# Performance work log

Hardware: AMD Instinct MI355X
Metric: run time of the kernel (lower is better)

The kernel has to match this reference:

```python
import jax, jax.numpy as jnp
import numpy as np

T = 48; S = 48; H = 250; EMB = 300; VOCAB = 50000; NL = 5


def setup_inputs():
    key = jax.random.key(0)
    ks = jax.random.split(key, 32)
    def rn(k, shape, scale=0.05):
        return jax.random.normal(k, shape, dtype=jnp.float32) * scale
    return {
        "x1": jax.random.randint(ks[0], (T,), 0, VOCAB),
        "x2": jax.random.randint(ks[1], (S,), 0, VOCAB),
        "emb": rn(ks[2], (VOCAB, EMB), 1.0),
        "w_ih_f": rn(ks[3], (4 * H, EMB)),
        "w_hh_f": rn(ks[4], (4 * H, H)),
        "b_f": rn(ks[5], (4 * H,)),
        "w_ih_b": rn(ks[6], (4 * H, EMB)),
        "w_hh_b": rn(ks[7], (4 * H, H)),
        "b_b": rn(ks[8], (4 * H,)),
        "c1_w": rn(ks[9], (128, 13, 3, 3)),  "c1_b": rn(ks[10], (128,)),
        "c2_w": rn(ks[11], (164, 128, 3, 3)), "c2_b": rn(ks[12], (164,)),
        "c3_w": rn(ks[13], (192, 164, 3, 3)), "c3_b": rn(ks[14], (192,)),
        "c4_w": rn(ks[15], (192, 192, 3, 3)), "c4_b": rn(ks[16], (192,)),
        "c5_w": rn(ks[17], (128, 192, 3, 3)), "c5_b": rn(ks[18], (128,)),
        "dnn_w": rn(ks[19], (128, 128)), "dnn_b": rn(ks[20], (128,)),
        "out_w": rn(ks[21], (NL, 128)), "out_b": rn(ks[22], (NL,)),
    }


def _lstm_dir(xW, w_hh, b, reverse):
    # xW: [T, 4H] precomputed input projection
    def cell(carry, g_in):
        h, c = carry
        g = g_in + h @ w_hh.T + b
        i, f, gg, o = jnp.split(g, 4)
        i = jax.nn.sigmoid(i); f = jax.nn.sigmoid(f)
        gg = jnp.tanh(gg); o = jax.nn.sigmoid(o)
        c = f * c + i * gg
        h = o * jnp.tanh(c)
        return (h, c), h
    h0 = jnp.zeros((w_hh.shape[1],), xW.dtype)
    _, hs = jax.lax.scan(cell, (h0, h0), xW, reverse=reverse)
    return hs  # [T, H], aligned to input positions


def _bilstm(x, w_ih_f, w_hh_f, b_f, w_ih_b, w_hh_b, b_b):
    hf = _lstm_dir(x @ w_ih_f.T, w_hh_f, b_f, False)
    hb = _lstm_dir(x @ w_ih_b.T, w_hh_b, b_b, True)
    return jnp.stack([hf, hb], axis=1)  # [T, 2, H]


def _sim(a, b):
    # a:[T,D], b:[S,D] -> [3,T,S] channels (dot, cos, l2) -- fully batched
    dot = a @ b.T
    na = jnp.sqrt(jnp.sum(a * a, -1))
    nb = jnp.sqrt(jnp.sum(b * b, -1))
    cos = dot / (na[:, None] * nb[None, :] + 1e-8)
    d2 = jnp.maximum(na[:, None] ** 2 + nb[None, :] ** 2 - 2.0 * dot, 1e-12)
    l2 = jnp.sqrt(d2)
    return jnp.stack([dot, cos, l2], 0)


def _sim_cube(seq1, seq2):
    h1f, h1b = seq1[:, 0], seq1[:, 1]
    h2f, h2b = seq2[:, 0], seq2[:, 1]
    parts = [
        _sim(jnp.concatenate([h1f, h1b], -1), jnp.concatenate([h2f, h2b], -1)),
        _sim(h1f, h2f),
        _sim(h1b, h2b),
        _sim(h1f + h1b, h2f + h2b),
    ]
    pad = jnp.zeros((1, seq1.shape[0], seq2.shape[0]), seq1.dtype)  # channel 12
    return jnp.concatenate(parts + [pad], 0)  # [13, T, S]


def _greedy_select(plane):
    # greedy non-conflicting pair selection over top (T+S) entries
    t, s = plane.shape
    _, idx = jax.lax.top_k(plane.reshape(-1), t + s)
    def step(carry, i):
        s1, s2, m = carry
        p1 = i // t  # faithful to original (divides by len(s1tag))
        p2 = i % s
        ok = (s1[p1] + s2[p2]) == 0
        s1 = s1.at[p1].set(jnp.where(ok, 1, s1[p1]))
        s2 = s2.at[p2].set(jnp.where(ok, 1, s2[p2]))
        m = m.at[p1, p2].set(m[p1, p2] | ok)
        return (s1, s2, m), None
    init = (jnp.zeros(t, jnp.int32), jnp.zeros(s, jnp.int32), jnp.zeros((t, s), bool))
    (_, _, m), _ = jax.lax.scan(step, init, idx)
    return m


def _focus_cube(sc):
    sel = _greedy_select(sc[10]) | _greedy_select(sc[11])
    mask = jnp.where(sel[None], 1.0, 0.1).astype(sc.dtype)  # 0.1 base per VDPWI
    mask = mask.at[12].set(1.0)
    return mask * sc


def _convnet(x, c1_w, c1_b, c2_w, c2_b, c3_w, c3_b, c4_w, c4_b, c5_w, c5_b,
             dnn_w, dnn_b, out_w, out_b):
    def conv(x, w, b):
        y = jax.lax.conv_general_dilated(
            x, w, (1, 1), ((1, 1), (1, 1)),
            dimension_numbers=("NCHW", "OIHW", "NCHW"))
        return y + b[None, :, None, None]
    def pool(x, k, st):
        return jax.lax.reduce_window(
            x, -jnp.inf, jax.lax.max, (1, 1, k, k), (1, 1, st, st), "VALID")
    x = pool(jax.nn.relu(conv(x, c1_w, c1_b)), 2, 2)  # 48->24
    x = pool(jax.nn.relu(conv(x, c2_w, c2_b)), 2, 2)  # 24->12
    x = pool(jax.nn.relu(conv(x, c3_w, c3_b)), 2, 2)  # 12->6
    x = pool(jax.nn.relu(conv(x, c4_w, c4_b)), 2, 2)  # 6->3
    x = pool(jax.nn.relu(conv(x, c5_w, c5_b)), 3, 1)  # 3->1
    x = x.reshape(x.shape[0], -1)  # [1, 128]
    x = jax.nn.relu(x @ dnn_w.T + dnn_b)
    return x @ out_w.T + out_b


def reference(x1, x2, emb, w_ih_f, w_hh_f, b_f, w_ih_b, w_hh_b, b_b,
              c1_w, c1_b, c2_w, c2_b, c3_w, c3_b, c4_w, c4_b, c5_w, c5_b,
              dnn_w, dnn_b, out_w, out_b):
    e1 = emb[x1]  # [T, 300]
    e2 = emb[x2]  # [S, 300]
    seq1 = _bilstm(e1, w_ih_f, w_hh_f, b_f, w_ih_b, w_hh_b, b_b)
    seq2 = _bilstm(e2, w_ih_f, w_hh_f, b_f, w_ih_b, w_hh_b, b_b)
    sc = _sim_cube(seq1, seq2)        # [13, T, S]
    fc = _focus_cube(sc)
    logits = _convnet(fc[None], c1_w, c1_b, c2_w, c2_b, c3_w, c3_b,
                      c4_w, c4_b, c5_w, c5_b, dnn_w, dnn_b, out_w, out_b)
    return jax.nn.log_softmax(logits, axis=-1)
```

## Files before the change

kernel.cpp:

```cpp
#include <hip/hip_runtime.h>
#include <math.h>


typedef __attribute__((ext_vector_type(2))) _Float16 h2f;
typedef unsigned long long u64;

#define OFF_XW    0
#define OFF_HS    192000
#define OFF_SC    240000
#define OFF_BUFA  269952
#define OFF_BUFB  343680
#define OFF_WIHT  367296
#define OFF_WPK   967296
#define OFF_SEL   1217296

__device__ __forceinline__ float sigf(float x) { return 1.f / (1.f + expf(-x)); }

#if __has_builtin(__builtin_amdgcn_fdot2)
__device__ __forceinline__ float dot2(h2f a, h2f b, float c) {
    return __builtin_amdgcn_fdot2(a, b, c, false);
}
#else
__device__ __forceinline__ float dot2(h2f a, h2f b, float c) {
    return c + (float)a.x * (float)b.x + (float)a.y * (float)b.y;
}
#endif

__global__ void prep_kernel(const float* __restrict__ wihf, const float* __restrict__ wihb,
                            const float* __restrict__ whhf, const float* __restrict__ whhb,
                            float* __restrict__ wT, unsigned int* __restrict__ wpk)
{
    if (blockIdx.z < 2) {
        __shared__ float tile[32][33];
        int dir = blockIdx.z;
        const float* w = dir ? wihb : wihf;

        int j = blockIdx.x * 32 + threadIdx.y;
        int k = blockIdx.y * 32 + threadIdx.x;
        if (j < 1000 && k < 300)
            tile[threadIdx.y][threadIdx.x] = w[(size_t)j * 300 + k];
        __syncthreads();

        int ko = blockIdx.y * 32 + threadIdx.y;
        int jo = blockIdx.x * 32 + threadIdx.x;
        if (ko < 300 && jo < 1000)
            wT[(size_t)dir * 300000 + (size_t)ko * 1000 + jo] = tile[threadIdx.x][threadIdx.y];
    } else {
        if (blockIdx.y >= 8) return;
        __shared__ unsigned int ptile[32][33];
        int jt  = blockIdx.x;
        int pt  = blockIdx.y & 3;
        int dir = blockIdx.y >> 2;
        const float* w = dir ? whhb : whhf;

        int p = pt * 32 + threadIdx.x;
        int j = jt * 32 + threadIdx.y;
        if (p < 125 && j < 1000) {
            float2 v = *(const float2*)(w + (size_t)j * 250 + 2 * p);
            h2f pv; pv.x = (_Float16)v.x; pv.y = (_Float16)v.y;
            ptile[threadIdx.y][threadIdx.x] = *(unsigned int*)&pv;
        }
        __syncthreads();

        int jo = jt * 32 + threadIdx.x;
        int po = pt * 32 + threadIdx.y;
        if (po < 125 && jo < 1000)
            wpk[(size_t)dir * 125000 + (size_t)po * 1000 + jo] = ptile[threadIdx.x][threadIdx.y];
    }
}

__global__ void embed_xw_kernel(const int* __restrict__ x1, const int* __restrict__ x2,
                                const float* __restrict__ emb, const float* __restrict__ wT,
                                const float* __restrict__ b_f, const float* __restrict__ b_b,
                                float* __restrict__ xW)
{
    int t = blockIdx.x % 48;
    int m = blockIdx.x / 48;
    const int* x = (m < 2) ? x1 : x2;
    const float* w = wT + (size_t)(m & 1) * 300000;
    const float* bias = (m & 1) ? b_b : b_f;

    __shared__ float e[300];
    int row = x[t];
    for (int k = threadIdx.x; k < 300; k += 512)
        e[k] = emb[(size_t)row * 300 + k];
    __syncthreads();

    int j0 = threadIdx.x;
    int j1 = threadIdx.x + 512;
    int j1c = j1 < 1000 ? j1 : 999;
    float a0 = 0.f, a1 = 0.f;
    #pragma unroll 4
    for (int k = 0; k < 300; ++k) {
        float ek = e[k];
        const float* wr = w + (size_t)k * 1000;
        a0 += ek * wr[j0];
        a1 += ek * wr[j1c];
    }
    float* out = xW + ((size_t)m * 48 + t) * 1000;
    out[j0] = a0 + bias[j0];
    if (j1 < 1000) out[j1] = a1 + bias[j1];
}

__global__ void __launch_bounds__(512, 1) lstm_kernel(
    const float* __restrict__ xW, const unsigned int* __restrict__ wpk,
    float* __restrict__ hs)
{
    int m   = blockIdx.x;
    int dir = m & 1;
    const unsigned int* wp = wpk + (size_t)dir * 125000;
    const float* xw = xW + (size_t)m * 48000;
    float* out      = hs + (size_t)m * 12000;

    int t = threadIdx.x;
    bool active = t < 500;
    int r0 = t, r1 = t + 500;

    __shared__ __align__(16) unsigned int hp[128];
    __shared__ float fo_lds[500];
    __shared__ __align__(16) uint4 wl4[3 * 1000];

    for (int idx = t; idx < 3000; idx += 512) {
        int q = idx / 1000, r = idx % 1000;
        uint4 v;
        v.x = wp[(4 * q + 0) * 1000 + r];
        v.y = wp[(4 * q + 1) * 1000 + r];
        v.z = wp[(4 * q + 2) * 1000 + r];
        v.w = wp[(4 * q + 3) * 1000 + r];
        wl4[idx] = v;
    }

    h2f w0r[113], w1r[113];
    if (active) {
        #pragma unroll
        for (int p = 0; p < 113; ++p) {
            unsigned int a = wp[(p + 12) * 1000 + r0];
            unsigned int b = wp[(p + 12) * 1000 + r1];
            w0r[p] = *(h2f*)&a;
            w1r[p] = *(h2f*)&b;
        }
    }
    if (t < 128) hp[t] = 0u;
    float c = 0.f;

    int tt = dir ? 47 : 0;
    float px0 = 0.f, px1 = 0.f;
    if (active) {
        px0 = xw[tt * 1000 + r0];
        px1 = xw[tt * 1000 + r1];
    }
    __syncthreads();

    for (int step = 0; step < 48; ++step) {
        int ttn = dir ? 46 - step : step + 1;
        float n0 = 0.f, n1 = 0.f;
        if (active && step < 47) {
            n0 = xw[ttn * 1000 + r0];
            n1 = xw[ttn * 1000 + r1];
        }
        float a0 = 0.f, a1 = 0.f;
        if (active) {
            float a0e = px0, a0o = 0.f, a1e = px1, a1o = 0.f;
            const uint4* hp4 = (const uint4*)hp;
            #pragma unroll
            for (int q = 0; q < 3; ++q) {
                uint4 hq = hp4[q];
                h2f h0 = *(h2f*)&hq.x, h1 = *(h2f*)&hq.y, h2v = *(h2f*)&hq.z, h3 = *(h2f*)&hq.w;
                uint4 wv0 = wl4[q * 1000 + r0];
                uint4 wv1 = wl4[q * 1000 + r1];
                a0e = dot2(*(h2f*)&wv0.x, h0, a0e);  a1e = dot2(*(h2f*)&wv1.x, h0, a1e);
                a0o = dot2(*(h2f*)&wv0.y, h1, a0o);  a1o = dot2(*(h2f*)&wv1.y, h1, a1o);
                a0e = dot2(*(h2f*)&wv0.z, h2v, a0e); a1e = dot2(*(h2f*)&wv1.z, h2v, a1e);
                a0o = dot2(*(h2f*)&wv0.w, h3, a0o);  a1o = dot2(*(h2f*)&wv1.w, h3, a1o);
            }
            #pragma unroll
            for (int jj = 3; jj < 31; ++jj) {
                uint4 hq = hp4[jj];
                h2f h0 = *(h2f*)&hq.x, h1 = *(h2f*)&hq.y, h2v = *(h2f*)&hq.z, h3 = *(h2f*)&hq.w;
                int p = 4 * jj - 12;
                a0e = dot2(w0r[p + 0], h0, a0e);  a1e = dot2(w1r[p + 0], h0, a1e);
                a0o = dot2(w0r[p + 1], h1, a0o);  a1o = dot2(w1r[p + 1], h1, a1o);
                a0e = dot2(w0r[p + 2], h2v, a0e); a1e = dot2(w1r[p + 2], h2v, a1e);
                a0o = dot2(w0r[p + 3], h3, a0o);  a1o = dot2(w1r[p + 3], h3, a1o);
            }
            {
                unsigned int hq = hp[124];
                h2f hv = *(h2f*)&hq;
                a0e = dot2(w0r[112], hv, a0e);
                a1e = dot2(w1r[112], hv, a1e);
            }
            a0 = a0e + a0o;
            a1 = a1e + a1o;
            if (t >= 250) {
                fo_lds[t - 250] = sigf(a0);
                fo_lds[250 + (t - 250)] = sigf(a1);
            }
        }
        __syncthreads();
        if (t < 250) {
            float iv = sigf(a0);
            float gv = tanhf(a1);
            float fv = fo_lds[t];
            float ov = fo_lds[250 + t];
            c = fv * c + iv * gv;
            float hn = ov * tanhf(c);
            out[tt * 250 + t] = hn;
            float hi = __shfl_down(hn, 1);
            if (!(t & 1)) {
                h2f pv; pv.x = (_Float16)hn; pv.y = (_Float16)hi;
                hp[t >> 1] = *(unsigned int*)&pv;
            }
        }
        px0 = n0; px1 = n1; tt = ttn;
        __syncthreads();
    }
}

__global__ void sim_kernel(const float* __restrict__ hs, float* __restrict__ sc)
{
    int p = blockIdx.x;
    int i = p / 48, jj = p % 48;
    const float* h1f = hs + ((size_t)0 * 48 + i) * 250;
    const float* h1b = hs + ((size_t)1 * 48 + i) * 250;
    const float* h2f = hs + ((size_t)2 * 48 + jj) * 250;
    const float* h2b = hs + ((size_t)3 * 48 + jj) * 250;
    int lane = threadIdx.x;
    float dff = 0.f, dbb = 0.f, dfb = 0.f, dbf = 0.f;
    float sfa = 0.f, sba = 0.f, caa = 0.f;
    float sfb = 0.f, sbb = 0.f, cbb = 0.f;
    for (int k = lane; k < 250; k += 64) {
        float af = h1f[k], ab = h1b[k], bf = h2f[k], bb = h2b[k];
        dff += af * bf; dbb += ab * bb; dfb += af * bb; dbf += ab * bf;
        sfa += af * af; sba += ab * ab; caa += af * ab;
        sfb += bf * bf; sbb += bb * bb; cbb += bf * bb;
    }
    #pragma unroll
    for (int o = 32; o; o >>= 1) {
        dff += __shfl_down(dff, o); dbb += __shfl_down(dbb, o);
        dfb += __shfl_down(dfb, o); dbf += __shfl_down(dbf, o);
        sfa += __shfl_down(sfa, o); sba += __shfl_down(sba, o);
        caa += __shfl_down(caa, o);
        sfb += __shfl_down(sfb, o); sbb += __shfl_down(sbb, o);
        cbb += __shfl_down(cbb, o);
    }
    if (lane == 0) {
        #define EMIT(basep, dotv, sa2, sb2)                                 \
        {                                                                   \
            float na = sqrtf(sa2), nbv = sqrtf(sb2);                        \
            float dv = (dotv);                                              \
            sc[(basep) * 2304 + p] = dv;                                    \
            sc[((basep) + 1) * 2304 + p] = dv / (na * nbv + 1e-8f);         \
            float d2 = fmaxf(na * na + nbv * nbv - 2.f * dv, 1e-12f);       \
            sc[((basep) + 2) * 2304 + p] = sqrtf(d2);                       \
        }
        EMIT(0, dff + dbb, sfa + sba, sfb + sbb);
        EMIT(3, dff, sfa, sfb);
        EMIT(6, dbb, sba, sbb);
        EMIT(9, dff + dfb + dbf + dbb, sfa + sba + 2.f * caa, sfb + sbb + 2.f * cbb);
        #undef EMIT
    }
}

__global__ void greedy_kernel(const float* __restrict__ sc, unsigned char* __restrict__ sel)
{
    __shared__ unsigned char selL[2304];
    int lane = threadIdx.x;
    int plane = 10 + blockIdx.x;

    u64 v[36];
    #pragma unroll
    for (int q = 0; q < 36; ++q) {
        int i = lane + 64 * q;
        unsigned int u = __float_as_uint(sc[plane * 2304 + i]);
        unsigned int ord = (u & 0x80000000u) ? ~u : (u | 0x80000000u);
        v[q] = ((u64)ord << 32) | (unsigned int)(4095 - i);
        selL[i] = 0;
    }

    #pragma unroll
    for (int a = 0; a < 35; ++a) {
        #pragma unroll
        for (int b = 0; b < 35 - a; ++b) {
            u64 lo = v[b] < v[b + 1] ? v[b] : v[b + 1];
            u64 hi = v[b] < v[b + 1] ? v[b + 1] : v[b];
            v[b] = hi; v[b + 1] = lo;
        }
    }
    __syncthreads();

    u64 m1 = 0, m2 = 0;
    for (int it = 0; it < 96; ++it) {
        u64 bv = v[0];
        #pragma unroll
        for (int o = 1; o < 64; o <<= 1) {
            u64 ov = __shfl_xor(bv, o);
            if (ov > bv) bv = ov;
        }
        int idx = 4095 - (int)(bv & 0xFFFFFFFFu);
        int p1 = idx / 48, p2 = idx % 48;
        bool ok = !((m1 >> p1) & 1) && !((m2 >> p2) & 1);
        if (ok) { m1 |= 1ull << p1; m2 |= 1ull << p2; }
        if (v[0] == bv) {
            if (ok) selL[idx] = 1;
            #pragma unroll
            for (int q = 0; q < 35; ++q) v[q] = v[q + 1];
            v[35] = 0;
        }
    }
    __syncthreads();
    for (int q = 0; q < 36; ++q) {
        int i = lane + 64 * q;
        sel[blockIdx.x * 2304 + i] = selL[i];
    }
}

__global__ void conv1_pool_kernel(const float* __restrict__ sc, const unsigned char* __restrict__ sel,
                                  const float* __restrict__ w, const float* __restrict__ bias,
                                  float* __restrict__ out)
{
    __shared__ float tile[256];
    int co  = blockIdx.x / 9;
    int tl  = blockIdx.x % 9;
    int ty0 = (tl / 3) * 16, tx0 = (tl % 3) * 16;
    int tx = threadIdx.x % 16, ty = threadIdx.x / 16;
    int x = tx0 + tx, y = ty0 + ty;

    float mv[9];
    #pragma unroll
    for (int ky = 0; ky < 3; ++ky) {
        int iy = y + ky - 1;
        #pragma unroll
        for (int kx = 0; kx < 3; ++kx) {
            int ix = x + kx - 1;
            float mm = 0.f;
            if (iy >= 0 && iy < 48 && ix >= 0 && ix < 48) {
                int p = iy * 48 + ix;
                mm = (sel[p] | sel[2304 + p]) ? 1.0f : 0.1f;
            }
            mv[ky * 3 + kx] = mm;
        }
    }

    float acc = bias[co];
    const float* wco = w + (size_t)co * 13 * 9;
    for (int ci = 0; ci < 12; ++ci) {
        const float* inp = sc + (size_t)ci * 2304;
        const float* wp = wco + ci * 9;
        #pragma unroll
        for (int ky = 0; ky < 3; ++ky) {
            int iy = y + ky - 1;
            if (iy < 0 || iy >= 48) continue;
            #pragma unroll
            for (int kx = 0; kx < 3; ++kx) {
                int ix = x + kx - 1;
                if (ix < 0 || ix >= 48) continue;
                acc += inp[iy * 48 + ix] * mv[ky * 3 + kx] * wp[ky * 3 + kx];
            }
        }
    }
    tile[threadIdx.x] = acc > 0.f ? acc : 0.f;
    __syncthreads();
    if (threadIdx.x < 64) {
        int py = threadIdx.x / 8, px = threadIdx.x % 8;
        float a = tile[(py * 2) * 16 + px * 2];
        float b = tile[(py * 2) * 16 + px * 2 + 1];
        float cc = tile[(py * 2 + 1) * 16 + px * 2];
        float d = tile[(py * 2 + 1) * 16 + px * 2 + 1];
        float best = fmaxf(fmaxf(a, b), fmaxf(cc, d));
        out[(size_t)co * 576 + (ty0 / 2 + py) * 24 + (tx0 / 2 + px)] = best;
    }
}

__global__ void conv_cs_kernel(const float* __restrict__ in, const float* __restrict__ w,
                               const float* __restrict__ bias, float* __restrict__ out,
                               int Cin, int H, int W, int tileH, int tileW,
                               int cpc, int CC, int pk, int ps, int PHf, int PWf)
{
    extern __shared__ float sm[];
    int P = tileH * tileW;
    int co = blockIdx.x;
    int ty0 = blockIdx.y * tileH, tx0 = blockIdx.z * tileW;
    int t = threadIdx.x;
    int pix = t % P, chunk = t / P;
    int y = ty0 + pix / tileW, x = tx0 + pix % tileW;
    int c0 = chunk * cpc;
    int c1 = c0 + cpc; if (c1 > Cin) c1 = Cin;

    float acc = 0.f;
    const float* wco = w + (size_t)co * Cin * 9;
    for (int ci = c0; ci < c1; ++ci) {
        const float* inp = in + (size_t)ci * H * W;
        const float* wp = wco + (size_t)ci * 9;
        #pragma unroll
        for (int ky = 0; ky < 3; ++ky) {
            int iy = y + ky - 1;
            if (iy < 0 || iy >= H) continue;
            const float* rowp = inp + iy * W;
            #pragma unroll
            for (int kx = 0; kx < 3; ++kx) {
                int ix = x + kx - 1;
                if (ix < 0 || ix >= W) continue;
                acc += rowp[ix] * wp[ky * 3 + kx];
            }
        }
    }
    sm[t] = acc;
    __syncthreads();
    float* res = sm + P * CC;
    if (chunk == 0) {
        float tot = bias[co];
        for (int cc2 = 0; cc2 < CC; ++cc2) tot += sm[pix + cc2 * P];
        res[pix] = tot > 0.f ? tot : 0.f;
    }
    __syncthreads();
    int pH = (tileH - pk) / ps + 1, pW = (tileW - pk) / ps + 1;
    if (t < pH * pW) {
        int py = t / pW, px = t % pW;
        float best = -INFINITY;
        for (int dy = 0; dy < pk; ++dy)
            for (int dx = 0; dx < pk; ++dx) {
                float v = res[(py * ps + dy) * tileW + (px * ps + dx)];
                best = v > best ? v : best;
            }
        out[((size_t)co * PHf + (ty0 / ps + py)) * PWf + (tx0 / ps + px)] = best;
    }
}

__global__ void head_kernel(const float* __restrict__ feat,
                            const float* __restrict__ dnn_w, const float* __restrict__ dnn_b,
                            const float* __restrict__ out_w, const float* __restrict__ out_b,
                            float* __restrict__ out)
{
    __shared__ float y[128];
    __shared__ float logits[5];
    int j = threadIdx.x;
    float acc = dnn_b[j];
    for (int k = 0; k < 128; ++k) acc += feat[k] * dnn_w[j * 128 + k];
    y[j] = acc > 0.f ? acc : 0.f;
    __syncthreads();
    if (j < 5) {
        float a = out_b[j];
        for (int k = 0; k < 128; ++k) a += y[k] * out_w[j * 128 + k];
        logits[j] = a;
    }
    __syncthreads();
    if (j == 0) {
        float m = logits[0];
        for (int l = 1; l < 5; ++l) m = fmaxf(m, logits[l]);
        float s = 0.f;
        for (int l = 0; l < 5; ++l) s += expf(logits[l] - m);
        float lse = logf(s);
        for (int l = 0; l < 5; ++l) out[l] = logits[l] - m - lse;
    }
}

extern "C" void kernel_launch(void* const* d_in, const int* in_sizes, int n_in,
                              void* d_out, int out_size, void* d_ws, size_t ws_size,
                              hipStream_t stream)
{
    const int*   x1     = (const int*)d_in[0];
    const int*   x2     = (const int*)d_in[1];
    const float* emb    = (const float*)d_in[2];
    const float* w_ih_f = (const float*)d_in[3];
    const float* w_hh_f = (const float*)d_in[4];
    const float* b_f    = (const float*)d_in[5];
    const float* w_ih_b = (const float*)d_in[6];
    const float* w_hh_b = (const float*)d_in[7];
    const float* b_b    = (const float*)d_in[8];
    const float* c1_w   = (const float*)d_in[9];
    const float* c1_b   = (const float*)d_in[10];
    const float* c2_w   = (const float*)d_in[11];
    const float* c2_b   = (const float*)d_in[12];
    const float* c3_w   = (const float*)d_in[13];
    const float* c3_b   = (const float*)d_in[14];
    const float* c4_w   = (const float*)d_in[15];
    const float* c4_b   = (const float*)d_in[16];
    const float* c5_w   = (const float*)d_in[17];
    const float* c5_b   = (const float*)d_in[18];
    const float* dnn_w  = (const float*)d_in[19];
    const float* dnn_b  = (const float*)d_in[20];
    const float* out_w  = (const float*)d_in[21];
    const float* out_b  = (const float*)d_in[22];

    float* ws    = (float*)d_ws;
    float* xW    = ws + OFF_XW;
    float* hsb   = ws + OFF_HS;
    float* sc    = ws + OFF_SC;
    float* bufA  = ws + OFF_BUFA;
    float* bufB  = ws + OFF_BUFB;
    float* wihT  = ws + OFF_WIHT;
    unsigned int* wpk = (unsigned int*)(ws + OFF_WPK);
    unsigned char* sel = (unsigned char*)(ws + OFF_SEL);
    float* outp  = (float*)d_out;

    prep_kernel<<<dim3(32, 10, 3), dim3(32, 32), 0, stream>>>(
        w_ih_f, w_ih_b, w_hh_f, w_hh_b, wihT, wpk);
    embed_xw_kernel<<<192, 512, 0, stream>>>(x1, x2, emb, wihT, b_f, b_b, xW);
    lstm_kernel<<<4, 512, 0, stream>>>(xW, wpk, hsb);
    sim_kernel<<<2304, 64, 0, stream>>>(hsb, sc);
    greedy_kernel<<<2, 64, 0, stream>>>(sc, sel);

    conv1_pool_kernel<<<128 * 9, 256, 0, stream>>>(sc, sel, c1_w, c1_b, bufA);
    conv_cs_kernel<<<dim3(164, 2, 2), 576, (576 + 144) * 4, stream>>>(
        bufA, c2_w, c2_b, bufB, 128, 24, 24, 12, 12, 32, 4, 2, 2, 12, 12);
    conv_cs_kernel<<<dim3(192, 1, 1), 576, (576 + 144) * 4, stream>>>(
        bufB, c3_w, c3_b, bufA, 164, 12, 12, 12, 12, 41, 4, 2, 2, 6, 6);
    conv_cs_kernel<<<dim3(192, 1, 1), 576, (576 + 36) * 4, stream>>>(
        bufA, c4_w, c4_b, bufB, 192, 6, 6, 6, 6, 12, 16, 2, 2, 3, 3);
    conv_cs_kernel<<<dim3(128, 1, 1), 576, (576 + 9) * 4, stream>>>(
        bufB, c5_w, c5_b, bufA, 192, 3, 3, 3, 3, 3, 64, 3, 1, 1, 1);

    head_kernel<<<1, 128, 0, stream>>>(bufA, dnn_w, dnn_b, out_w, out_b, outp);
}
```

Baseline: 345.6 us.

## Fuse sim, greedy, conv stack and head into one persistent kernel with grid barriers

Eight separate launches (similarity, greedy matching, five conv/pool layers, head) become a single persistent kernel of 256 blocks. The stages are separated by atomic-counter grid barriers, and the counter is reset in prep_kernel. The aim is to remove per-launch overhead and the gaps between the many tiny kernels that follow the LSTM. In exchange, the greedy stage runs while most blocks spin at a barrier, and correctness depends on all 256 blocks being co-resident.

```diff
diff --git a/kernel.cpp b/kernel.cpp
--- a/kernel.cpp
+++ b/kernel.cpp
@@ -13,6 +13,9 @@
 #define OFF_WIHT  367296
 #define OFF_WPK   967296
 #define OFF_SEL   1217296
+#define OFF_CNT   1218448
+
+#define NBLK 256
 
 __device__ __forceinline__ float sigf(float x) { return 1.f / (1.f + expf(-x)); }
 
@@ -26,10 +29,28 @@
 }
 #endif
 
+__device__ __forceinline__ void gridbar(int* cnt, int target) {
+    __syncthreads();
+    if (threadIdx.x == 0) {
+        __hip_atomic_fetch_add(cnt, 1, __ATOMIC_ACQ_REL, __HIP_MEMORY_SCOPE_AGENT);
+        while (__hip_atomic_load(cnt, __ATOMIC_ACQUIRE, __HIP_MEMORY_SCOPE_AGENT) < target) {
+#if __has_builtin(__builtin_amdgcn_s_sleep)
+            __builtin_amdgcn_s_sleep(2);
+#endif
+        }
+    }
+    __syncthreads();
+}
+
 __global__ void prep_kernel(const float* __restrict__ wihf, const float* __restrict__ wihb,
                             const float* __restrict__ whhf, const float* __restrict__ whhb,
-                            float* __restrict__ wT, unsigned int* __restrict__ wpk)
+                            float* __restrict__ wT, unsigned int* __restrict__ wpk,
+                            int* __restrict__ cnt)
 {
+    if (blockIdx.x == 0 && blockIdx.y == 0 && blockIdx.z == 0 &&
+        threadIdx.x == 0 && threadIdx.y == 0)
+        __hip_atomic_store(cnt, 0, __ATOMIC_RELAXED, __HIP_MEMORY_SCOPE_AGENT);
+
     if (blockIdx.z < 2) {
         __shared__ float tile[32][33];
         int dir = blockIdx.z;
@@ -216,241 +237,270 @@
     }
 }
 
-__global__ void sim_kernel(const float* __restrict__ hs, float* __restrict__ sc)
+__device__ __forceinline__ void conv_tile(const float* __restrict__ in, const float* __restrict__ w,
+    const float* __restrict__ bias, float* __restrict__ out, float* sm, int t, bool act,
+    int Cin, int H, int W, int tileH, int tileW, int ty0, int tx0,
+    int cpc, int CC, int pk, int ps, int PHf, int PWf, int co)
 {
-    int p = blockIdx.x;
-    int i = p / 48, jj = p % 48;
-    const float* h1f = hs + ((size_t)0 * 48 + i) * 250;
-    const float* h1b = hs + ((size_t)1 * 48 + i) * 250;
-    const float* h2f = hs + ((size_t)2 * 48 + jj) * 250;
-    const float* h2b = hs + ((size_t)3 * 48 + jj) * 250;
-    int lane = threadIdx.x;
-    float dff = 0.f, dbb = 0.f, dfb = 0.f, dbf = 0.f;
-    float sfa = 0.f, sba = 0.f, caa = 0.f;
-    float sfb = 0.f, sbb = 0.f, cbb = 0.f;
-    for (int k = lane; k < 250; k += 64) {
-        float af = h1f[k], ab = h1b[k], bf = h2f[k], bb = h2b[k];
-        dff += af * bf; dbb += ab * bb; dfb += af * bb; dbf += ab * bf;
-        sfa += af * af; sba += ab * ab; caa += af * ab;
-        sfb += bf * bf; sbb += bb * bb; cbb += bf * bb;
-    }
-    #pragma unroll
-    for (int o = 32; o; o >>= 1) {
-        dff += __shfl_down(dff, o); dbb += __shfl_down(dbb, o);
-        dfb += __shfl_down(dfb, o); dbf += __shfl_down(dbf, o);
-        sfa += __shfl_down(sfa, o); sba += __shfl_down(sba, o);
-        caa += __shfl_down(caa, o);
-        sfb += __shfl_down(sfb, o); sbb += __shfl_down(sbb, o);
-        cbb += __shfl_down(cbb, o);
-    }
-    if (lane == 0) {
-        #define EMIT(basep, dotv, sa2, sb2)                                 \
-        {                                                                   \
-            float na = sqrtf(sa2), nbv = sqrtf(sb2);                        \
-            float dv = (dotv);                                              \
-            sc[(basep) * 2304 + p] = dv;                                    \
-            sc[((basep) + 1) * 2304 + p] = dv / (na * nbv + 1e-8f);         \
-            float d2 = fmaxf(na * na + nbv * nbv - 2.f * dv, 1e-12f);       \
-            sc[((basep) + 2) * 2304 + p] = sqrtf(d2);                       \
-        }
-        EMIT(0, dff + dbb, sfa + sba, sfb + sbb);
-        EMIT(3, dff, sfa, sfb);
-        EMIT(6, dbb, sba, sbb);
-        EMIT(9, dff + dfb + dbf + dbb, sfa + sba + 2.f * caa, sfb + sbb + 2.f * cbb);
-        #undef EMIT
-    }
-}
-
-__global__ void greedy_kernel(const float* __restrict__ sc, unsigned char* __restrict__ sel)
-{
-    __shared__ unsigned char selL[2304];
-    int lane = threadIdx.x;
-    int plane = 10 + blockIdx.x;
-
-    u64 v[36];
-    #pragma unroll
-    for (int q = 0; q < 36; ++q) {
-        int i = lane + 64 * q;
-        unsigned int u = __float_as_uint(sc[plane * 2304 + i]);
-        unsigned int ord = (u & 0x80000000u) ? ~u : (u | 0x80000000u);
-        v[q] = ((u64)ord << 32) | (unsigned int)(4095 - i);
-        selL[i] = 0;
-    }
-
-    #pragma unroll
-    for (int a = 0; a < 35; ++a) {
-        #pragma unroll
-        for (int b = 0; b < 35 - a; ++b) {
-            u64 lo = v[b] < v[b + 1] ? v[b] : v[b + 1];
-            u64 hi = v[b] < v[b + 1] ? v[b + 1] : v[b];
-            v[b] = hi; v[b + 1] = lo;
-        }
-    }
-    __syncthreads();
-
-    u64 m1 = 0, m2 = 0;
-    for (int it = 0; it < 96; ++it) {
-        u64 bv = v[0];
-        #pragma unroll
-        for (int o = 1; o < 64; o <<= 1) {
-            u64 ov = __shfl_xor(bv, o);
-            if (ov > bv) bv = ov;
-        }
-        int idx = 4095 - (int)(bv & 0xFFFFFFFFu);
-        int p1 = idx / 48, p2 = idx % 48;
-        bool ok = !((m1 >> p1) & 1) && !((m2 >> p2) & 1);
-        if (ok) { m1 |= 1ull << p1; m2 |= 1ull << p2; }
-        if (v[0] == bv) {
-            if (ok) selL[idx] = 1;
-            #pragma unroll
-            for (int q = 0; q < 35; ++q) v[q] = v[q + 1];
-            v[35] = 0;
-        }
-    }
-    __syncthreads();
-    for (int q = 0; q < 36; ++q) {
-        int i = lane + 64 * q;
-        sel[blockIdx.x * 2304 + i] = selL[i];
-    }
-}
-
-__global__ void conv1_pool_kernel(const float* __restrict__ sc, const unsigned char* __restrict__ sel,
-                                  const float* __restrict__ w, const float* __restrict__ bias,
-                                  float* __restrict__ out)
-{
-    __shared__ float tile[256];
-    int co  = blockIdx.x / 9;
-    int tl  = blockIdx.x % 9;
-    int ty0 = (tl / 3) * 16, tx0 = (tl % 3) * 16;
-    int tx = threadIdx.x % 16, ty = threadIdx.x / 16;
-    int x = tx0 + tx, y = ty0 + ty;
-
-    float mv[9];
-    #pragma unroll
-    for (int ky = 0; ky < 3; ++ky) {
-        int iy = y + ky - 1;
-        #pragma unroll
-        for (int kx = 0; kx < 3; ++kx) {
-            int ix = x + kx - 1;
-            float mm = 0.f;
-            if (iy >= 0 && iy < 48 && ix >= 0 && ix < 48) {
-                int p = iy * 48 + ix;
-                mm = (sel[p] | sel[2304 + p]) ? 1.0f : 0.1f;
-            }
-            mv[ky * 3 + kx] = mm;
-        }
-    }
-
-    float acc = bias[co];
-    const float* wco = w + (size_t)co * 13 * 9;
-    for (int ci = 0; ci < 12; ++ci) {
-        const float* inp = sc + (size_t)ci * 2304;
-        const float* wp = wco + ci * 9;
-        #pragma unroll
-        for (int ky = 0; ky < 3; ++ky) {
-            int iy = y + ky - 1;
-            if (iy < 0 || iy >= 48) continue;
-            #pragma unroll
-            for (int kx = 0; kx < 3; ++kx) {
-                int ix = x + kx - 1;
-                if (ix < 0 || ix >= 48) continue;
-                acc += inp[iy * 48 + ix] * mv[ky * 3 + kx] * wp[ky * 3 + kx];
-            }
-        }
-    }
-    tile[threadIdx.x] = acc > 0.f ? acc : 0.f;
-    __syncthreads();
-    if (threadIdx.x < 64) {
-        int py = threadIdx.x / 8, px = threadIdx.x % 8;
-        float a = tile[(py * 2) * 16 + px * 2];
-        float b = tile[(py * 2) * 16 + px * 2 + 1];
-        float cc = tile[(py * 2 + 1) * 16 + px * 2];
-        float d = tile[(py * 2 + 1) * 16 + px * 2 + 1];
-        float best = fmaxf(fmaxf(a, b), fmaxf(cc, d));
-        out[(size_t)co * 576 + (ty0 / 2 + py) * 24 + (tx0 / 2 + px)] = best;
-    }
-}
-
-__global__ void conv_cs_kernel(const float* __restrict__ in, const float* __restrict__ w,
-                               const float* __restrict__ bias, float* __restrict__ out,
-                               int Cin, int H, int W, int tileH, int tileW,
-                               int cpc, int CC, int pk, int ps, int PHf, int PWf)
-{
-    extern __shared__ float sm[];
     int P = tileH * tileW;
-    int co = blockIdx.x;
-    int ty0 = blockIdx.y * tileH, tx0 = blockIdx.z * tileW;
-    int t = threadIdx.x;
     int pix = t % P, chunk = t / P;
     int y = ty0 + pix / tileW, x = tx0 + pix % tileW;
-    int c0 = chunk * cpc;
-    int c1 = c0 + cpc; if (c1 > Cin) c1 = Cin;
-
     float acc = 0.f;
-    const float* wco = w + (size_t)co * Cin * 9;
-    for (int ci = c0; ci < c1; ++ci) {
-        const float* inp = in + (size_t)ci * H * W;
-        const float* wp = wco + (size_t)ci * 9;
-        #pragma unroll
-        for (int ky = 0; ky < 3; ++ky) {
-            int iy = y + ky - 1;
-            if (iy < 0 || iy >= H) continue;
-            const float* rowp = inp + iy * W;
+    if (act && chunk < CC) {
+        int c0 = chunk * cpc, c1 = c0 + cpc; if (c1 > Cin) c1 = Cin;
+        const float* wco = w + (size_t)co * Cin * 9;
+        for (int ci = c0; ci < c1; ++ci) {
+            const float* inp = in + (size_t)ci * H * W;
+            const float* wp = wco + (size_t)ci * 9;
             #pragma unroll
-            for (int kx = 0; kx < 3; ++kx) {
-                int ix = x + kx - 1;
-                if (ix < 0 || ix >= W) continue;
-                acc += rowp[ix] * wp[ky * 3 + kx];
+            for (int ky = 0; ky < 3; ++ky) {
+                int iy = y + ky - 1;
+                if (iy < 0 || iy >= H) continue;
+                const float* rowp = inp + iy * W;
+                #pragma unroll
+                for (int kx = 0; kx < 3; ++kx) {
+                    int ix = x + kx - 1;
+                    if (ix < 0 || ix >= W) continue;
+                    acc += rowp[ix] * wp[ky * 3 + kx];
+                }
             }
         }
     }
     sm[t] = acc;
     __syncthreads();
-    float* res = sm + P * CC;
-    if (chunk == 0) {
+    if (act && chunk == 0) {
         float tot = bias[co];
         for (int cc2 = 0; cc2 < CC; ++cc2) tot += sm[pix + cc2 * P];
-        res[pix] = tot > 0.f ? tot : 0.f;
+        sm[576 + pix] = tot > 0.f ? tot : 0.f;
     }
     __syncthreads();
     int pH = (tileH - pk) / ps + 1, pW = (tileW - pk) / ps + 1;
-    if (t < pH * pW) {
+    if (act && t < pH * pW) {
         int py = t / pW, px = t % pW;
         float best = -INFINITY;
         for (int dy = 0; dy < pk; ++dy)
             for (int dx = 0; dx < pk; ++dx) {
-                float v = res[(py * ps + dy) * tileW + (px * ps + dx)];
+                float v = sm[576 + (py * ps + dy) * tileW + (px * ps + dx)];
                 best = v > best ? v : best;
             }
         out[((size_t)co * PHf + (ty0 / ps + py)) * PWf + (tx0 / ps + px)] = best;
     }
-}
-
-__global__ void head_kernel(const float* __restrict__ feat,
-                            const float* __restrict__ dnn_w, const float* __restrict__ dnn_b,
-                            const float* __restrict__ out_w, const float* __restrict__ out_b,
-                            float* __restrict__ out)
+    __syncthreads();
+}
+
+__global__ void __launch_bounds__(576) tail_kernel(
+    const float* __restrict__ hs, float* __restrict__ sc, unsigned char* __restrict__ sel,
+    const float* __restrict__ c1_w, const float* __restrict__ c1_b,
+    const float* __restrict__ c2_w, const float* __restrict__ c2_b,
+    const float* __restrict__ c3_w, const float* __restrict__ c3_b,
+    const float* __restrict__ c4_w, const float* __restrict__ c4_b,
+    const float* __restrict__ c5_w, const float* __restrict__ c5_b,
+    const float* __restrict__ dnn_w, const float* __restrict__ dnn_b,
+    const float* __restrict__ out_w, const float* __restrict__ out_b,
+    float* __restrict__ bufA, float* __restrict__ bufB,
+    int* __restrict__ cnt, float* __restrict__ outp)
 {
-    __shared__ float y[128];
-    __shared__ float logits[5];
-    int j = threadIdx.x;
-    float acc = dnn_b[j];
-    for (int k = 0; k < 128; ++k) acc += feat[k] * dnn_w[j * 128 + k];
-    y[j] = acc > 0.f ? acc : 0.f;
-    __syncthreads();
-    if (j < 5) {
-        float a = out_b[j];
-        for (int k = 0; k < 128; ++k) a += y[k] * out_w[j * 128 + k];
-        logits[j] = a;
-    }
-    __syncthreads();
-    if (j == 0) {
-        float m = logits[0];
-        for (int l = 1; l < 5; ++l) m = fmaxf(m, logits[l]);
+    __shared__ float sm[720];
+    __shared__ unsigned char selL[2304];
+    int t = threadIdx.x;
+    int b = blockIdx.x;
+
+    {
+        int wave = t >> 6, lane = t & 63;
+        int p = b * 9 + wave;
+        int i = p / 48, jj = p % 48;
+        const float* h1f = hs + ((size_t)0 * 48 + i) * 250;
+        const float* h1b = hs + ((size_t)1 * 48 + i) * 250;
+        const float* h2f = hs + ((size_t)2 * 48 + jj) * 250;
+        const float* h2b = hs + ((size_t)3 * 48 + jj) * 250;
+        float dff = 0.f, dbb = 0.f, dfb = 0.f, dbf = 0.f;
+        float sfa = 0.f, sba = 0.f, caa = 0.f;
+        float sfb = 0.f, sbb = 0.f, cbb = 0.f;
+        for (int k = lane; k < 250; k += 64) {
+            float af = h1f[k], ab = h1b[k], bf = h2f[k], bb = h2b[k];
+            dff += af * bf; dbb += ab * bb; dfb += af * bb; dbf += ab * bf;
+            sfa += af * af; sba += ab * ab; caa += af * ab;
+            sfb += bf * bf; sbb += bb * bb; cbb += bf * bb;
+        }
+        #pragma unroll
+        for (int o = 32; o; o >>= 1) {
+            dff += __shfl_down(dff, o); dbb += __shfl_down(dbb, o);
+            dfb += __shfl_down(dfb, o); dbf += __shfl_down(dbf, o);
+            sfa += __shfl_down(sfa, o); sba += __shfl_down(sba, o);
+            caa += __shfl_down(caa, o);
+            sfb += __shfl_down(sfb, o); sbb += __shfl_down(sbb, o);
+            cbb += __shfl_down(cbb, o);
+        }
+        if (lane == 0) {
+            #define EMIT(basep, dotv, sa2, sb2)                                 \
+            {                                                                   \
+                float na = sqrtf(sa2), nbv = sqrtf(sb2);                        \
+                float dv = (dotv);                                              \
+                sc[(basep) * 2304 + p] = dv;                                    \
+                sc[((basep) + 1) * 2304 + p] = dv / (na * nbv + 1e-8f);         \
+                float d2 = fmaxf(na * na + nbv * nbv - 2.f * dv, 1e-12f);       \
+                sc[((basep) + 2) * 2304 + p] = sqrtf(d2);                       \
+            }
+            EMIT(0, dff + dbb, sfa + sba, sfb + sbb);
+            EMIT(3, dff, sfa, sfb);
+            EMIT(6, dbb, sba, sbb);
+            EMIT(9, dff + dfb + dbf + dbb, sfa + sba + 2.f * caa, sfb + sbb + 2.f * cbb);
+            #undef EMIT
+        }
+    }
+    gridbar(cnt, NBLK * 1);
+
+    if (b < 2 && t < 64) {
+        int lane = t;
+        int plane = 10 + b;
+        u64 v[36];
+        #pragma unroll
+        for (int q = 0; q < 36; ++q) {
+            int i = lane + 64 * q;
+            unsigned int u = __float_as_uint(sc[plane * 2304 + i]);
+            unsigned int ord = (u & 0x80000000u) ? ~u : (u | 0x80000000u);
+            v[q] = ((u64)ord << 32) | (unsigned int)(4095 - i);
+            selL[i] = 0;
+        }
+        #pragma unroll
+        for (int a = 0; a < 35; ++a) {
+            #pragma unroll
+            for (int bb2 = 0; bb2 < 35 - a; ++bb2) {
+                u64 lo = v[bb2] < v[bb2 + 1] ? v[bb2] : v[bb2 + 1];
+                u64 hi = v[bb2] < v[bb2 + 1] ? v[bb2 + 1] : v[bb2];
+                v[bb2] = hi; v[bb2 + 1] = lo;
+            }
+        }
+        u64 m1 = 0, m2 = 0;
+        for (int it = 0; it < 96; ++it) {
+            u64 bv = v[0];
+            #pragma unroll
+            for (int o = 1; o < 64; o <<= 1) {
+                u64 ov = __shfl_xor(bv, o);
+                if (ov > bv) bv = ov;
+            }
+            int idx = 4095 - (int)(bv & 0xFFFFFFFFu);
+            int p1 = idx / 48, p2 = idx % 48;
+            bool ok = !((m1 >> p1) & 1) && !((m2 >> p2) & 1);
+            if (ok) { m1 |= 1ull << p1; m2 |= 1ull << p2; }
+            if (v[0] == bv) {
+                if (ok) selL[idx] = 1;
+                #pragma unroll
+                for (int q = 0; q < 35; ++q) v[q] = v[q + 1];
+                v[35] = 0;
+            }
+        }
+        for (int q = 0; q < 36; ++q) {
+            int i = lane + 64 * q;
+            sel[b * 2304 + i] = selL[i];
+        }
+    }
+    gridbar(cnt, NBLK * 2);
+
+    for (int iter = 0; iter < 3; ++iter) {
+        int sub = t >> 8;
+        int ltid = t & 255;
+        int job = iter * 512 + b * 2 + sub;
+        bool act = (sub < 2) && (job < 1152);
+        float r = 0.f;
+        int co = 0, ty0 = 0, tx0 = 0;
+        if (act) {
+            co = job / 9;
+            int tl = job % 9;
+            ty0 = (tl / 3) * 16; tx0 = (tl % 3) * 16;
+            int tx = ltid % 16, ty = ltid / 16;
+            int x = tx0 + tx, y = ty0 + ty;
+            float mv[9];
+            #pragma unroll
+            for (int ky = 0; ky < 3; ++ky) {
+                int iy = y + ky - 1;
+                #pragma unroll
+                for (int kx = 0; kx < 3; ++kx) {
+                    int ix = x + kx - 1;
+                    float mm = 0.f;
+                    if (iy >= 0 && iy < 48 && ix >= 0 && ix < 48) {
+                        int p = iy * 48 + ix;
+                        mm = (sel[p] | sel[2304 + p]) ? 1.0f : 0.1f;
+                    }
+                    mv[ky * 3 + kx] = mm;
+                }
+            }
+            float acc = c1_b[co];
+            const float* wco = c1_w + (size_t)co * 13 * 9;
+            for (int ci = 0; ci < 12; ++ci) {
+                const float* inp = sc + (size_t)ci * 2304;
+                const float* wp = wco + ci * 9;
+                #pragma unroll
+                for (int ky = 0; ky < 3; ++ky) {
+                    int iy = y + ky - 1;
+                    if (iy < 0 || iy >= 48) continue;
+                    #pragma unroll
+                    for (int kx = 0; kx < 3; ++kx) {
+                        int ix = x + kx - 1;
+                        if (ix < 0 || ix >= 48) continue;
+                        acc += inp[iy * 48 + ix] * mv[ky * 3 + kx] * wp[ky * 3 + kx];
+                    }
+                }
+            }
+            r = acc > 0.f ? acc : 0.f;
+        }
+        if (sub < 2) sm[sub * 256 + ltid] = r;
+        __syncthreads();
+        if (act && ltid < 64) {
+            int py = ltid / 8, px = ltid % 8;
+            float* tile = sm + sub * 256;
+            float a = tile[(py * 2) * 16 + px * 2];
+            float bb2 = tile[(py * 2) * 16 + px * 2 + 1];
+            float cc = tile[(py * 2 + 1) * 16 + px * 2];
+            float d = tile[(py * 2 + 1) * 16 + px * 2 + 1];
+            float best = fmaxf(fmaxf(a, bb2), fmaxf(cc, d));
+            bufA[(size_t)co * 576 + (ty0 / 2 + py) * 24 + (tx0 / 2 + px)] = best;
+        }
+        __syncthreads();
+    }
+    gridbar(cnt, NBLK * 3);
+
+    for (int iter = 0; iter < 3; ++iter) {
+        int job = iter * 256 + b;
+        bool act = job < 656;
+        int co = job >> 2, tyi = (job >> 1) & 1, txi = job & 1;
+        conv_tile(bufA, c2_w, c2_b, bufB, sm, t, act,
+                  128, 24, 24, 12, 12, tyi * 12, txi * 12, 32, 4, 2, 2, 12, 12, co);
+    }
+    gridbar(cnt, NBLK * 4);
+
+    conv_tile(bufB, c3_w, c3_b, bufA, sm, t, b < 192,
+              164, 12, 12, 12, 12, 0, 0, 41, 4, 2, 2, 6, 6, b);
+    gridbar(cnt, NBLK * 5);
+
+    conv_tile(bufA, c4_w, c4_b, bufB, sm, t, b < 192,
+              192, 6, 6, 6, 6, 0, 0, 12, 16, 2, 2, 3, 3, b);
+    gridbar(cnt, NBLK * 6);
+
+    conv_tile(bufB, c5_w, c5_b, bufA, sm, t, b < 128,
+              192, 3, 3, 3, 3, 0, 0, 3, 64, 3, 1, 1, 1, b);
+    gridbar(cnt, NBLK * 7);
+
+    if (b != 0) return;
+    if (t < 128) {
+        float a = dnn_b[t];
+        for (int k = 0; k < 128; ++k) a += bufA[k] * dnn_w[t * 128 + k];
+        sm[t] = a > 0.f ? a : 0.f;
+    }
+    __syncthreads();
+    if (t < 5) {
+        float a = out_b[t];
+        for (int k = 0; k < 128; ++k) a += sm[k] * out_w[t * 128 + k];
+        sm[128 + t] = a;
+    }
+    __syncthreads();
+    if (t == 0) {
+        float mx = sm[128];
+        for (int l = 1; l < 5; ++l) mx = fmaxf(mx, sm[128 + l]);
         float s = 0.f;
-        for (int l = 0; l < 5; ++l) s += expf(logits[l] - m);
+        for (int l = 0; l < 5; ++l) s += expf(sm[128 + l] - mx);
         float lse = logf(s);
-        for (int l = 0; l < 5; ++l) out[l] = logits[l] - m - lse;
+        for (int l = 0; l < 5; ++l) outp[l] = sm[128 + l] - mx - lse;
     }
 }
 
@@ -491,24 +541,14 @@
     float* wihT  = ws + OFF_WIHT;
     unsigned int* wpk = (unsigned int*)(ws + OFF_WPK);
     unsigned char* sel = (unsigned char*)(ws + OFF_SEL);
+    int*   cnt   = (int*)(ws + OFF_CNT);
     float* outp  = (float*)d_out;
 
     prep_kernel<<<dim3(32, 10, 3), dim3(32, 32), 0, stream>>>(
-        w_ih_f, w_ih_b, w_hh_f, w_hh_b, wihT, wpk);
+        w_ih_f, w_ih_b, w_hh_f, w_hh_b, wihT, wpk, cnt);
     embed_xw_kernel<<<192, 512, 0, stream>>>(x1, x2, emb, wihT, b_f, b_b, xW);
     lstm_kernel<<<4, 512, 0, stream>>>(xW, wpk, hsb);
-    sim_kernel<<<2304, 64, 0, stream>>>(hsb, sc);
-    greedy_kernel<<<2, 64, 0, stream>>>(sc, sel);
-
-    conv1_pool_kernel<<<128 * 9, 256, 0, stream>>>(sc, sel, c1_w, c1_b, bufA);
-    conv_cs_kernel<<<dim3(164, 2, 2), 576, (576 + 144) * 4, stream>>>(
-        bufA, c2_w, c2_b, bufB, 128, 24, 24, 12, 12, 32, 4, 2, 2, 12, 12);
-    conv_cs_kernel<<<dim3(192, 1, 1), 576, (576 + 144) * 4, stream>>>(
-        bufB, c3_w, c3_b, bufA, 164, 12, 12, 12, 12, 41, 4, 2, 2, 6, 6);
-    conv_cs_kernel<<<dim3(192, 1, 1), 576, (576 + 36) * 4, stream>>>(
-        bufA, c4_w, c4_b, bufB, 192, 6, 6, 6, 6, 12, 16, 2, 2, 3, 3);
-    conv_cs_kernel<<<dim3(128, 1, 1), 576, (576 + 9) * 4, stream>>>(
-        bufB, c5_w, c5_b, bufA, 192, 3, 3, 3, 3, 3, 64, 3, 1, 1, 1);
-
-    head_kernel<<<1, 128, 0, stream>>>(bufA, dnn_w, dnn_b, out_w, out_b, outp);
-}
+    tail_kernel<<<NBLK, 576, 0, stream>>>(
+        hsb, sc, sel, c1_w, c1_b, c2_w, c2_b, c3_w, c3_b, c4_w, c4_b, c5_w, c5_b,
+        dnn_w, dnn_b, out_w, out_b, bufA, bufB, cnt, outp);
+}
```

Result: slower. 669.2 us (+93.6%).
